# Kernel optimization log

Measured on AMD Instinct MI355X. Metric: run time of the kernel, lower is better.

Reference implementation:

```python
import jax, jax.numpy as jnp
import numpy as np

D = 1024      # embedding_size
H = 16        # num_heads
HD = D // H   # head_size
EPS = 1e-5


def setup_inputs() -> dict:
    key = jax.random.key(0)
    ks = jax.random.split(key, 12)
    s_in = 1.0 / np.sqrt(D)
    s_hid = 1.0 / np.sqrt(4 * D)
    return {
        "x": jax.random.normal(ks[0], (2, 2048, D), dtype=jnp.float32),
        # per-head projections, no bias: [H, D, HD]
        "Wq": jax.random.normal(ks[1], (H, D, HD), dtype=jnp.float32) * s_in,
        "Wk": jax.random.normal(ks[2], (H, D, HD), dtype=jnp.float32) * s_in,
        "Wv": jax.random.normal(ks[3], (H, D, HD), dtype=jnp.float32) * s_in,
        "Wo": jax.random.normal(ks[4], (D, D), dtype=jnp.float32) * s_in,
        "bo": jnp.zeros((D,), dtype=jnp.float32),
        "W1": jax.random.normal(ks[5], (D, 4 * D), dtype=jnp.float32) * s_in,
        "b1": jnp.zeros((4 * D,), dtype=jnp.float32),
        "W2": jax.random.normal(ks[6], (4 * D, D), dtype=jnp.float32) * s_hid,
        "b2": jnp.zeros((D,), dtype=jnp.float32),
        "g1": jnp.ones((D,), dtype=jnp.float32),
        "be1": jnp.zeros((D,), dtype=jnp.float32),
        "g2": jnp.ones((D,), dtype=jnp.float32),
        "be2": jnp.zeros((D,), dtype=jnp.float32),
    }


def _layernorm(x, g, b):
    mu = jnp.mean(x, axis=-1, keepdims=True)
    var = jnp.mean(jnp.square(x - mu), axis=-1, keepdims=True)
    return (x - mu) * jax.lax.rsqrt(var + EPS) * g + b


def _block(x, Wq, Wk, Wv, Wo, bo, W1, b1, W2, b2, g1, be1, g2, be2):
    B, T, _ = x.shape
    h = _layernorm(x, g1, be1)
    # per-head projections: [B, H, T, HD]
    q = jnp.einsum('btd,hde->bhte', h, Wq)
    k = jnp.einsum('btd,hde->bhte', h, Wk)
    v = jnp.einsum('btd,hde->bhte', h, Wv)
    # NOTE: original scales by embedding_size**-0.5 (x.shape[-1]), not head_size
    scores = jnp.einsum('bhte,bhse->bhts', q, k) * (D ** -0.5)
    mask = jnp.tril(jnp.ones((T, T), dtype=bool))
    scores = jnp.where(mask, scores, -jnp.inf)
    attn = jax.nn.softmax(scores, axis=-1)           # dropout = identity (eval)
    out = jnp.einsum('bhts,bhse->bhte', attn, v)      # [B, H, T, HD]
    out = out.transpose(0, 2, 1, 3).reshape(B, T, D)  # concat heads
    x = x + (out @ Wo + bo)
    h2 = _layernorm(x, g2, be2)
    ffn = jax.nn.relu(h2 @ W1 + b1) @ W2 + b2
    return x + ffn


def reference(x, Wq, Wk, Wv, Wo, bo, W1, b1, W2, b2, g1, be1, g2, be2):
    return _block(x, Wq, Wk, Wv, Wo, bo, W1, b1, W2, b2, g1, be1, g2, be2)
```

## Files before the change

kernel.cpp:

```cpp
#include <hip/hip_runtime.h>
#include <stdint.h>

typedef unsigned short u16;
typedef __attribute__((ext_vector_type(8))) __bf16 bf16x8;
typedef __attribute__((ext_vector_type(4))) float f32x4;

#define D_EMB 1024
#define NHEAD 16
#define HDIM 64
#define TSEQ 2048
#define NTOK 4096
#define NEG_BIG -1.0e30f

#define GLD16(lp, gp) __builtin_amdgcn_global_load_lds( \
    (const __attribute__((address_space(1))) unsigned int*)(gp), \
    (__attribute__((address_space(3))) unsigned int*)(lp), 16, 0, 0)

__device__ __forceinline__ float bf2f(u16 u) {
    union { unsigned int i; float f; } c; c.i = ((unsigned int)u) << 16; return c.f;
}
__device__ __forceinline__ u16 f2bf(float f) {
    union { float f; unsigned int i; } c; c.f = f;
    unsigned int r = (c.i + 0x7FFFu + ((c.i >> 16) & 1u)) >> 16;
    return (u16)r;
}
__device__ __forceinline__ void cp16(u16* dst, const u16* src) {
    *reinterpret_cast<uint4*>(dst) = *reinterpret_cast<const uint4*>(src);
}
__device__ __forceinline__ float load_in(const u16* p, size_t idx, int f32) {
    return f32 ? reinterpret_cast<const float*>(p)[idx] : bf2f(p[idx]);
}
__device__ __forceinline__ size_t tidx(int row, int col, int KB) {
    int c = (col & 7) | ((((col >> 3) ^ row) & 3) << 3);
    return ((size_t)((row >> 7) * KB + (col >> 5)) * 128 + (row & 127)) * 32 + c;
}

__global__ void detect_kernel(const u16* __restrict__ x, u16* __restrict__ fl) {
    if (threadIdx.x == 0) {
        int f = 0;
        for (int i = 0; i < 128; ++i) {
            float v = fabsf(bf2f(x[i]));
            if (!(v <= 1.0e3f)) f = 1;
        }
        fl[0] = (u16)f;
    }
}

__global__ __launch_bounds__(256) void transpose_tiled_kernel(
        const u16* __restrict__ X, u16* __restrict__ Xt, int KB,
        const u16* __restrict__ fl) {
    __shared__ __align__(16) u16 Ts[64 * 72];
    int f32 = fl[0];
    int bi = blockIdx.y, bj = blockIdx.x;
    int NS = gridDim.x * 64;
    int t = threadIdx.x;
    for (int p = 0; p < 2; ++p) {
        int idx = p * 256 + t;
        int row = idx >> 3, col8 = (idx & 7) * 8;
        size_t src = (size_t)(bi * 64 + row) * NS + bj * 64 + col8;
        if (f32) {
            for (int jj = 0; jj < 8; ++jj)
                Ts[row * 72 + col8 + jj] = f2bf(reinterpret_cast<const float*>(X)[src + jj]);
        } else {
            cp16(&Ts[row * 72 + col8], &X[src]);
        }
    }
    __syncthreads();
    for (int p = 0; p < 2; ++p) {
        int idx = p * 256 + t;
        int row = idx >> 3, col8 = (idx & 7) * 8;
        union { u16 u[8]; uint4 v; } tmp;
        for (int jj = 0; jj < 8; ++jj) tmp.u[jj] = Ts[(col8 + jj) * 72 + row];
        int n = bj * 64 + row, k0 = bi * 64 + col8;
        *reinterpret_cast<uint4*>(&Xt[tidx(n, k0, KB)]) = tmp.v;
    }
}

__global__ __launch_bounds__(256) void pack_qkv_kernel(
        const u16* __restrict__ Wq, const u16* __restrict__ Wk,
        const u16* __restrict__ Wv, u16* __restrict__ Wt,
        const u16* __restrict__ fl) {
    int f32 = fl[0];
    int idx = blockIdx.x * 256 + threadIdx.x;
    int e = idx & 63, d = (idx >> 6) & 1023, hh = (idx >> 16) & 15, sel = idx >> 20;
    const u16* W = (sel == 0) ? Wq : ((sel == 1) ? Wk : Wv);
    size_t src = (size_t)hh * (D_EMB * HDIM) + (size_t)d * HDIM + e;
    float v = f32 ? reinterpret_cast<const float*>(W)[src] : bf2f(W[src]);
    int n = sel * 1024 + hh * 64 + e;
    Wt[tidx(n, d, 32)] = f2bf(v);
}

__global__ __launch_bounds__(256) void ln_kernel(
        const u16* __restrict__ X, const u16* __restrict__ g,
        const u16* __restrict__ be, u16* __restrict__ Ht,
        const u16* __restrict__ fl) {
    int f32 = fl[0];
    int row = blockIdx.x;
    int t = threadIdx.x;
    float v[4];
    float s = 0.f, sq = 0.f;
    for (int i = 0; i < 4; ++i) {
        v[i] = load_in(X, (size_t)row * D_EMB + t + i * 256, f32);
        s += v[i]; sq += v[i] * v[i];
    }
    for (int m = 32; m; m >>= 1) { s += __shfl_down(s, m); sq += __shfl_down(sq, m); }
    __shared__ float red[8];
    int wid = t >> 6, lane = t & 63;
    if (lane == 0) { red[wid] = s; red[wid + 4] = sq; }
    __syncthreads();
    if (t == 0) {
        float S = red[0] + red[1] + red[2] + red[3];
        float SQ = red[4] + red[5] + red[6] + red[7];
        float mean = S * (1.f / 1024.f);
        float var = SQ * (1.f / 1024.f) - mean * mean;
        red[0] = mean; red[1] = rsqrtf(var + 1e-5f);
    }
    __syncthreads();
    float mean = red[0], rstd = red[1];
    for (int i = 0; i < 4; ++i) {
        int c = t + i * 256;
        float hv = (v[i] - mean) * rstd * load_in(g, c, f32) + load_in(be, c, f32);
        Ht[tidx(row, c, 32)] = f2bf(hv);
    }
}

template<int TAG, int TN>
__global__ __launch_bounds__(256) void gemm_t(
        const u16* __restrict__ At, const u16* __restrict__ Bt, u16* __restrict__ C,
        const u16* __restrict__ bias, const u16* __restrict__ res,
        int N, int K, int flags, int row_off,
        const u16* __restrict__ fl) {
    constexpr int NF = (TN == 128) ? 4 : 2;
    __shared__ __align__(16) u16 As2[2][4096];
    __shared__ __align__(16) u16 Bs2[2][TN * 32];
    int f32 = fl[0];
    int t = threadIdx.x;
    int gx = gridDim.x, gy = gridDim.y;
    int id = blockIdx.y * gx + blockIdx.x;
    int total = gx * gy;
    int xcd = id & 7, seq = id >> 3, P = total >> 3;
    int tpb = (P >= 32) ? 32 : 16;
    int th  = (P >= 32) ? 8 : 4;
    int tile = xcd * (P / tpb) + seq / tpb;
    int within = seq % tpb;
    int tiles_x = gx >> 2;
    int bx = (tile % tiles_x) * 4 + (within & 3);
    int by = (tile / tiles_x) * th + (within >> 2);
    int n0 = bx * TN, m0 = by * 128;
    int w = t >> 6, lane = t & 63, quad = lane >> 4, l16 = lane & 15;
    int wm = (TN == 128) ? (w >> 1) * 64 : (w & 1) * 64;
    int wn = (TN == 128) ? (w & 1) * 64  : (w >> 1) * 32;
    int KB = K >> 5;
    int kb0 = (seq * (KB >> 5)) & (KB - 1);
    const u16* Ab = At + (size_t)(m0 >> 7) * KB * 4096 + w * 512 + lane * 8;
    const u16* Bb = Bt + (size_t)(n0 >> 7) * KB * 4096
                       + ((TN == 64) ? (n0 & 64) * 32 : 0) + w * 512 + lane * 8;

    auto stage = [&](int buf, int kb) {
        const u16* ga = Ab + (size_t)kb * 4096;
        const u16* gb = Bb + (size_t)kb * 4096;
        u16* la = &As2[buf][w * 512];
        u16* lb = &Bs2[buf][w * 512];
        GLD16(la, ga);
        GLD16(la + 2048, ga + 2048);
        GLD16(lb, gb);
        if constexpr (TN == 128) { GLD16(lb + 2048, gb + 2048); }
    };

    const f32x4 fz = {0.f, 0.f, 0.f, 0.f};
    f32x4 acc[4][NF];
    for (int mt = 0; mt < 4; ++mt)
        for (int nt = 0; nt < NF; ++nt) acc[mt][nt] = fz;

    stage(0, kb0);
    __syncthreads();
    int kb = kb0;
    for (int it = 0; it < KB; ++it) {
        int cur = it & 1;
        int kn = (kb + 1 == KB) ? 0 : kb + 1;
        if (it + 1 < KB) stage(cur ^ 1, kn);
        bf16x8 af[4], bfr[NF];
        for (int mt = 0; mt < 4; ++mt) {
            int r = wm + mt * 16 + l16;
            af[mt] = *reinterpret_cast<const bf16x8*>(
                &As2[cur][r * 32 + (((quad ^ r) & 3) << 3)]);
        }
        for (int nt = 0; nt < NF; ++nt) {
            int r = wn + nt * 16 + l16;
            bfr[nt] = *reinterpret_cast<const bf16x8*>(
                &Bs2[cur][r * 32 + (((quad ^ r) & 3) << 3)]);
        }
        for (int mt = 0; mt < 4; ++mt)
            for (int nt = 0; nt < NF; ++nt)
                acc[mt][nt] = __builtin_amdgcn_mfma_f32_16x16x32_bf16(af[mt], bfr[nt], acc[mt][nt], 0, 0, 0);
        __syncthreads();
        kb = kn;
    }

    int relu_f = flags & 1, out_ext = flags & 2, c_tiled = flags & 4;
    for (int mt = 0; mt < 4; ++mt)
        for (int nt = 0; nt < NF; ++nt)
            for (int r = 0; r < 4; ++r) {
                int gr = m0 + wm + mt * 16 + quad * 4 + r;
                int gc = n0 + wn + nt * 16 + l16;
                float v = acc[mt][nt][r];
                if (bias) v += load_in(bias, gc, f32);
                if (relu_f) v = v > 0.f ? v : 0.f;
                size_t oidx = (size_t)(row_off + gr) * N + gc;
                if (res) v += load_in(res, oidx, f32);
                if (c_tiled)      C[tidx(gr, gc, N >> 5)] = f2bf(v);
                else if (out_ext && f32) reinterpret_cast<float*>(C)[oidx] = v;
                else              C[oidx] = f2bf(v);
            }
}

template<int TAG, int KBL, int TN>
__global__ __launch_bounds__(256) void gemm_sk_t(
        const u16* __restrict__ At, const u16* __restrict__ Bt,
        float* __restrict__ Pp, int N, int K) {
    constexpr int NF = (TN == 128) ? 4 : 2;
    __shared__ __align__(16) u16 As2[2][4096];
    __shared__ __align__(16) u16 Bs2[2][TN * 32];
    int t = threadIdx.x;
    int gx = gridDim.x, gy = gridDim.y;
    int id = blockIdx.y * gx + blockIdx.x;
    int total = gx * gy;
    int xcd = id & 7, seq = id >> 3, P = total >> 3;
    int tpb = (P >= 32) ? 32 : 16;
    int th  = (P >= 32) ? 8 : 4;
    int tile = xcd * (P / tpb) + seq / tpb;
    int within = seq % tpb;
    int tiles_x = gx >> 2;
    int bx = (tile % tiles_x) * 4 + (within & 3);
    int by = (tile / tiles_x) * th + (within >> 2);
    int n0 = bx * TN, m0 = by * 128;
    int w = t >> 6, lane = t & 63, quad = lane >> 4, l16 = lane & 15;
    int wm = (TN == 128) ? (w >> 1) * 64 : (w & 1) * 64;
    int wn = (TN == 128) ? (w & 1) * 64  : (w >> 1) * 32;
    int KB = K >> 5;
    int kstart = blockIdx.z * KBL;
    int rel0 = seq & (KBL - 1);
    const u16* Ab = At + (size_t)(m0 >> 7) * KB * 4096 + w * 512 + lane * 8;
    const u16* Bb = Bt + (size_t)(n0 >> 7) * KB * 4096
                       + ((TN == 64) ? (n0 & 64) * 32 : 0) + w * 512 + lane * 8;

    auto stage = [&](int buf, int kb) {
        const u16* ga = Ab + (size_t)kb * 4096;
        const u16* gb = Bb + (size_t)kb * 4096;
        u16* la = &As2[buf][w * 512];
        u16* lb = &Bs2[buf][w * 512];
        GLD16(la, ga);
        GLD16(la + 2048, ga + 2048);
        GLD16(lb, gb);
        if constexpr (TN == 128) { GLD16(lb + 2048, gb + 2048); }
    };

    const f32x4 fz = {0.f, 0.f, 0.f, 0.f};
    f32x4 acc[4][NF];
    for (int mt = 0; mt < 4; ++mt)
        for (int nt = 0; nt < NF; ++nt) acc[mt][nt] = fz;

    stage(0, kstart + rel0);
    __syncthreads();
    for (int it = 0; it < KBL; ++it) {
        int cur = it & 1;
        if (it + 1 < KBL)
            stage(cur ^ 1, kstart + ((rel0 + it + 1) & (KBL - 1)));
        bf16x8 af[4], bfr[NF];
        for (int mt = 0; mt < 4; ++mt) {
            int r = wm + mt * 16 + l16;
            af[mt] = *reinterpret_cast<const bf16x8*>(
                &As2[cur][r * 32 + (((quad ^ r) & 3) << 3)]);
        }
        for (int nt = 0; nt < NF; ++nt) {
            int r = wn + nt * 16 + l16;
            bfr[nt] = *reinterpret_cast<const bf16x8*>(
                &Bs2[cur][r * 32 + (((quad ^ r) & 3) << 3)]);
        }
        for (int mt = 0; mt < 4; ++mt)
            for (int nt = 0; nt < NF; ++nt)
                acc[mt][nt] = __builtin_amdgcn_mfma_f32_16x16x32_bf16(af[mt], bfr[nt], acc[mt][nt], 0, 0, 0);
        __syncthreads();
    }

    for (int mt = 0; mt < 4; ++mt)
        for (int nt = 0; nt < NF; ++nt)
            for (int r = 0; r < 4; ++r) {
                int gr = m0 + wm + mt * 16 + quad * 4 + r;
                int gc = n0 + wn + nt * 16 + l16;
                atomicAdd(&Pp[(size_t)gr * N + gc], acc[mt][nt][r]);
            }
}

__global__ __launch_bounds__(256) void zero_f32_kernel(float* __restrict__ p) {
    const f32x4 fz = {0.f, 0.f, 0.f, 0.f};
    reinterpret_cast<f32x4*>(p)[(size_t)blockIdx.x * 256 + threadIdx.x] = fz;
}

__global__ __launch_bounds__(256) void ffn_fin_kernel(
        const float* __restrict__ Pp, const u16* __restrict__ b2,
        u16* __restrict__ out, int row_off, const u16* __restrict__ fl) {
    int f32 = fl[0];
    size_t i = ((size_t)blockIdx.x * 256 + threadIdx.x) * 4;
    int col = (int)(i & 1023);
    f32x4 pv = *reinterpret_cast<const f32x4*>(Pp + i);
    size_t o = (size_t)row_off * 1024 + i;
    if (f32) {
        float* of = reinterpret_cast<float*>(out);
        f32x4 ov = *reinterpret_cast<f32x4*>(of + o);
        for (int j = 0; j < 4; ++j)
            ov[j] += pv[j] + load_in(b2, col + j, 1);
        *reinterpret_cast<f32x4*>(of + o) = ov;
    } else {
        for (int j = 0; j < 4; ++j) {
            float v = bf2f(out[o + j]) + pv[j] + bf2f(b2[col + j]);
            out[o + j] = f2bf(v);
        }
    }
}

__global__ __launch_bounds__(256) void oproj_fin_kernel(
        const float* __restrict__ Pp, const u16* __restrict__ bo,
        const u16* __restrict__ x, u16* __restrict__ out,
        const u16* __restrict__ fl) {
    int f32 = fl[0];
    size_t i = ((size_t)blockIdx.x * 256 + threadIdx.x) * 4;
    int col = (int)(i & 1023);
    f32x4 pv = *reinterpret_cast<const f32x4*>(Pp + i);
    if (f32) {
        const float* xf = reinterpret_cast<const float*>(x);
        float* of = reinterpret_cast<float*>(out);
        f32x4 ov;
        for (int j = 0; j < 4; ++j)
            ov[j] = xf[i + j] + pv[j] + load_in(bo, col + j, 1);
        *reinterpret_cast<f32x4*>(of + i) = ov;
    } else {
        for (int j = 0; j < 4; ++j) {
            float v = bf2f(x[i + j]) + pv[j] + bf2f(bo[col + j]);
            out[i + j] = f2bf(v);
        }
    }
}

__global__ __launch_bounds__(256) void flash_kernel(
        const u16* __restrict__ qkv, u16* __restrict__ attn_t) {
    __shared__ __align__(16) u16 Qs[64 * 72];
    __shared__ __align__(16) u16 Vs[64 * 72];
    __shared__ __align__(16) u16 Ps[64 * 72];
    int t = threadIdx.x;
    int tq = gridDim.x - 1 - blockIdx.x;
    int b = blockIdx.y >> 4, h = blockIdx.y & 15;
    int wid = t >> 6, lane = t & 63, quad = lane >> 4, l16 = lane & 15;
    const size_t seq_base = (size_t)b * TSEQ;

    for (int p = 0; p < 2; ++p) {
        int idx = p * 256 + t;
        int row = idx >> 3, col8 = (idx & 7) * 8;
        cp16(&Qs[row * 72 + col8],
             &qkv[(seq_base + tq * 64 + row) * 3072 + h * 64 + col8]);
    }

    const f32x4 fz = {0.f, 0.f, 0.f, 0.f};
    float m_run[4], l_run[4];
    f32x4 o[4];
    for (int r = 0; r < 4; ++r) { m_run[r] = NEG_BIG; l_run[r] = 0.f; }
    for (int nt = 0; nt < 4; ++nt) o[nt] = fz;

    for (int j = 0; j <= tq; ++j) {
        for (int p = 0; p < 2; ++p) {
            int idx = p * 256 + t;
            int row = idx >> 3, col8 = (idx & 7) * 8;
            cp16(&Vs[row * 72 + col8],
                 &qkv[(seq_base + j * 64 + row) * 3072 + 2048 + h * 64 + col8]);
        }
        __syncthreads();

        f32x4 sa[4];
        for (int nt = 0; nt < 4; ++nt) sa[nt] = fz;
        for (int kit = 0; kit < 2; ++kit) {
            bf16x8 aq = *reinterpret_cast<const bf16x8*>(
                &Qs[(wid * 16 + l16) * 72 + kit * 32 + quad * 8]);
            for (int nt = 0; nt < 4; ++nt) {
                bf16x8 bk = *reinterpret_cast<const bf16x8*>(
                    &qkv[(seq_base + j * 64 + nt * 16 + l16) * 3072 + 1024 + h * 64 + kit * 32 + quad * 8]);
                sa[nt] = __builtin_amdgcn_mfma_f32_16x16x32_bf16(aq, bk, sa[nt], 0, 0, 0);
            }
        }

        float p_val[4][4];
        int qbase = tq * 64 + wid * 16 + quad * 4;
        int sbase = j * 64 + l16;
        for (int r = 0; r < 4; ++r) {
            float sv[4];
            float mx = NEG_BIG;
            for (int nt = 0; nt < 4; ++nt) {
                float xv = sa[nt][r] * 0.03125f;
                if (sbase + nt * 16 > qbase + r) xv = NEG_BIG;
                sv[nt] = xv;
                mx = fmaxf(mx, xv);
            }
            for (int m = 1; m < 16; m <<= 1) mx = fmaxf(mx, __shfl_xor(mx, m));
            float mnew = fmaxf(m_run[r], mx);
            float alpha = __expf(m_run[r] - mnew);
            m_run[r] = mnew;
            float rs = 0.f;
            for (int nt = 0; nt < 4; ++nt) {
                float pv = __expf(sv[nt] - mnew);
                p_val[nt][r] = pv;
                rs += pv;
            }
            for (int m = 1; m < 16; m <<= 1) rs += __shfl_xor(rs, m);
            l_run[r] = l_run[r] * alpha + rs;
            for (int nt = 0; nt < 4; ++nt) o[nt][r] *= alpha;
        }

        for (int nt = 0; nt < 4; ++nt)
            for (int r = 0; r < 4; ++r)
                Ps[(wid * 16 + quad * 4 + r) * 72 + nt * 16 + l16] = f2bf(p_val[nt][r]);
        __syncthreads();

        for (int kit = 0; kit < 2; ++kit) {
            bf16x8 ap = *reinterpret_cast<const bf16x8*>(
                &Ps[(wid * 16 + l16) * 72 + kit * 32 + quad * 8]);
            for (int nt = 0; nt < 4; ++nt) {
                union { u16 u[8]; bf16x8 v; } bv;
                for (int jj = 0; jj < 8; ++jj)
                    bv.u[jj] = Vs[(kit * 32 + quad * 8 + jj) * 72 + nt * 16 + l16];
                o[nt] = __builtin_amdgcn_mfma_f32_16x16x32_bf16(ap, bv.v, o[nt], 0, 0, 0);
            }
        }
        __syncthreads();
    }

    for (int nt = 0; nt < 4; ++nt)
        for (int r = 0; r < 4; ++r) {
            int trow = (int)seq_base + tq * 64 + wid * 16 + quad * 4 + r;
            int col = h * 64 + nt * 16 + l16;
            attn_t[tidx(trow, col, 32)] = f2bf(o[nt][r] / l_run[r]);
        }
}

extern "C" void kernel_launch(void* const* d_in, const int* in_sizes, int n_in,
                              void* d_out, int out_size, void* d_ws, size_t ws_size,
                              hipStream_t stream) {
    const u16* x   = (const u16*)d_in[0];
    const u16* Wq  = (const u16*)d_in[1];
    const u16* Wk  = (const u16*)d_in[2];
    const u16* Wv  = (const u16*)d_in[3];
    const u16* Wo  = (const u16*)d_in[4];
    const u16* bo  = (const u16*)d_in[5];
    const u16* W1  = (const u16*)d_in[6];
    const u16* b1  = (const u16*)d_in[7];
    const u16* W2  = (const u16*)d_in[8];
    const u16* b2  = (const u16*)d_in[9];
    const u16* g1  = (const u16*)d_in[10];
    const u16* be1 = (const u16*)d_in[11];
    const u16* g2  = (const u16*)d_in[12];
    const u16* be2 = (const u16*)d_in[13];
    u16* out = (u16*)d_out;

    const size_t M1 = (size_t)1 << 20;
    u16* ws    = (u16*)d_ws;
    u16* qkv   = ws;
    u16* W2t   = ws;
    u16* a1    = ws + 4 * M1;
    u16* h     = ws + 12 * M1;
    u16* attn  = ws + 12 * M1;
    u16* h2    = ws + 12 * M1;
    u16* Wtq   = ws + 16 * M1;
    u16* Wot   = ws + 16 * M1;
    u16* W1t   = ws + 16 * M1;
    u16* fl    = ws + 20 * M1;
    float* Pp  = reinterpret_cast<float*>(ws + 21 * M1);
    bool sk = ws_size >= ((size_t)58 << 20);

    detect_kernel<<<1, 64, 0, stream>>>(x, fl);

    pack_qkv_kernel<<<(3 * 16 * 1024 * 64) / 256, 256, 0, stream>>>(Wq, Wk, Wv, Wtq, fl);
    ln_kernel<<<NTOK, 256, 0, stream>>>(x, g1, be1, h, fl);
    gemm_t<0, 64><<<dim3(48, 32), 256, 0, stream>>>(
        h, Wtq, qkv, nullptr, nullptr, 3072, 1024, 0, 0, fl);

    transpose_tiled_kernel<<<dim3(16, 16), 256, 0, stream>>>(Wo, Wot, 32, fl);

    flash_kernel<<<dim3(32, 32), 256, 0, stream>>>(qkv, attn);

    if (sk) {
        zero_f32_kernel<<<4096, 256, 0, stream>>>(Pp);
        gemm_sk_t<2, 8, 64><<<dim3(16, 32, 4), 256, 0, stream>>>(attn, Wot, Pp, 1024, 1024);
        oproj_fin_kernel<<<4096, 256, 0, stream>>>(Pp, bo, x, out, fl);
    } else {
        gemm_t<1, 128><<<dim3(8, 32), 256, 0, stream>>>(
            attn, Wot, out, bo, x, 1024, 1024, 2, 0, fl);
    }

    transpose_tiled_kernel<<<dim3(16, 64), 256, 0, stream>>>(W2, W2t, 128, fl);
    transpose_tiled_kernel<<<dim3(64, 16), 256, 0, stream>>>(W1, W1t, 32, fl);
    ln_kernel<<<NTOK, 256, 0, stream>>>(out, g2, be2, h2, fl);

    gemm_t<2, 64><<<dim3(64, 16), 256, 0, stream>>>(
        h2, W1t, a1, b1, nullptr, 4096, 1024, 1 | 4, 0, fl);
    if (sk) {
        zero_f32_kernel<<<2048, 256, 0, stream>>>(Pp);
        gemm_sk_t<0, 32, 64><<<dim3(16, 16, 4), 256, 0, stream>>>(a1, W2t, Pp, 1024, 4096);
        ffn_fin_kernel<<<2048, 256, 0, stream>>>(Pp, b2, out, 0, fl);
    } else {
        gemm_t<4, 128><<<dim3(8, 16), 256, 0, stream>>>(
            a1, W2t, out, b2, out, 1024, 4096, 2, 0, fl);
    }
    gemm_t<3, 64><<<dim3(64, 16), 256, 0, stream>>>(
        h2 + (size_t)2 * M1, W1t, a1, b1, nullptr, 4096, 1024, 1 | 4, 0, fl);
    if (sk) {
        zero_f32_kernel<<<2048, 256, 0, stream>>>(Pp);
        gemm_sk_t<1, 32, 64><<<dim3(16, 16, 4), 256, 0, stream>>>(a1, W2t, Pp, 1024, 4096);
        ffn_fin_kernel<<<2048, 256, 0, stream>>>(Pp, b2, out, 2048, fl);
    } else {
        gemm_t<5, 128><<<dim3(8, 16), 256, 0, stream>>>(
            a1, W2t, out, b2, out, 1024, 4096, 2, 2048, fl);
    }
}
```

Baseline: 662.3 us.

## Write V transposed from QKV GEMM and drop LDS staging in flash attention

```diff
diff --git a/kernel.cpp b/kernel.cpp
--- a/kernel.cpp
+++ b/kernel.cpp
@@ -127,6 +127,7 @@
 template<int TAG, int TN>
 __global__ __launch_bounds__(256) void gemm_t(
         const u16* __restrict__ At, const u16* __restrict__ Bt, u16* __restrict__ C,
+        u16* __restrict__ C2,
         const u16* __restrict__ bias, const u16* __restrict__ res,
         int N, int K, int flags, int row_off,
         const u16* __restrict__ fl) {
@@ -197,7 +198,7 @@
         kb = kn;
     }
 
-    int relu_f = flags & 1, out_ext = flags & 2, c_tiled = flags & 4;
+    int relu_f = flags & 1, out_ext = flags & 2, c_tiled = flags & 4, qkvsp = flags & 8;
     for (int mt = 0; mt < 4; ++mt)
         for (int nt = 0; nt < NF; ++nt)
             for (int r = 0; r < 4; ++r) {
@@ -208,7 +209,16 @@
                 if (relu_f) v = v > 0.f ? v : 0.f;
                 size_t oidx = (size_t)(row_off + gr) * N + gc;
                 if (res) v += load_in(res, oidx, f32);
-                if (c_tiled)      C[tidx(gr, gc, N >> 5)] = f2bf(v);
+                if (qkvsp) {
+                    if (gc < 2048) {
+                        C[(size_t)gr * 2048 + gc] = f2bf(v);
+                    } else {
+                        int hh = (gc - 2048) >> 6, d = gc & 63;
+                        int bb = gr >> 11, s = gr & 2047;
+                        C2[(((size_t)bb * 16 + hh) * 64 + d) * 2048 + s] = f2bf(v);
+                    }
+                }
+                else if (c_tiled)      C[tidx(gr, gc, N >> 5)] = f2bf(v);
                 else if (out_ext && f32) reinterpret_cast<float*>(C)[oidx] = v;
                 else              C[oidx] = f2bf(v);
             }
@@ -343,22 +353,20 @@
 }
 
 __global__ __launch_bounds__(256) void flash_kernel(
-        const u16* __restrict__ qkv, u16* __restrict__ attn_t) {
-    __shared__ __align__(16) u16 Qs[64 * 72];
-    __shared__ __align__(16) u16 Vs[64 * 72];
+        const u16* __restrict__ qk, const u16* __restrict__ vt,
+        u16* __restrict__ attn_t) {
     __shared__ __align__(16) u16 Ps[64 * 72];
     int t = threadIdx.x;
     int tq = gridDim.x - 1 - blockIdx.x;
     int b = blockIdx.y >> 4, h = blockIdx.y & 15;
     int wid = t >> 6, lane = t & 63, quad = lane >> 4, l16 = lane & 15;
     const size_t seq_base = (size_t)b * TSEQ;
-
-    for (int p = 0; p < 2; ++p) {
-        int idx = p * 256 + t;
-        int row = idx >> 3, col8 = (idx & 7) * 8;
-        cp16(&Qs[row * 72 + col8],
-             &qkv[(seq_base + tq * 64 + row) * 3072 + h * 64 + col8]);
-    }
+    const u16* vplane = vt + (size_t)(b * 16 + h) * 64 * 2048;
+
+    bf16x8 aq[2];
+    for (int kit = 0; kit < 2; ++kit)
+        aq[kit] = *reinterpret_cast<const bf16x8*>(
+            &qk[(seq_base + tq * 64 + wid * 16 + l16) * 2048 + h * 64 + kit * 32 + quad * 8]);
 
     const f32x4 fz = {0.f, 0.f, 0.f, 0.f};
     float m_run[4], l_run[4];
@@ -367,23 +375,13 @@
     for (int nt = 0; nt < 4; ++nt) o[nt] = fz;
 
     for (int j = 0; j <= tq; ++j) {
-        for (int p = 0; p < 2; ++p) {
-            int idx = p * 256 + t;
-            int row = idx >> 3, col8 = (idx & 7) * 8;
-            cp16(&Vs[row * 72 + col8],
-                 &qkv[(seq_base + j * 64 + row) * 3072 + 2048 + h * 64 + col8]);
-        }
-        __syncthreads();
-
         f32x4 sa[4];
         for (int nt = 0; nt < 4; ++nt) sa[nt] = fz;
         for (int kit = 0; kit < 2; ++kit) {
-            bf16x8 aq = *reinterpret_cast<const bf16x8*>(
-                &Qs[(wid * 16 + l16) * 72 + kit * 32 + quad * 8]);
             for (int nt = 0; nt < 4; ++nt) {
                 bf16x8 bk = *reinterpret_cast<const bf16x8*>(
-                    &qkv[(seq_base + j * 64 + nt * 16 + l16) * 3072 + 1024 + h * 64 + kit * 32 + quad * 8]);
-                sa[nt] = __builtin_amdgcn_mfma_f32_16x16x32_bf16(aq, bk, sa[nt], 0, 0, 0);
+                    &qk[(seq_base + j * 64 + nt * 16 + l16) * 2048 + 1024 + h * 64 + kit * 32 + quad * 8]);
+                sa[nt] = __builtin_amdgcn_mfma_f32_16x16x32_bf16(aq[kit], bk, sa[nt], 0, 0, 0);
             }
         }
 
@@ -417,19 +415,16 @@
         for (int nt = 0; nt < 4; ++nt)
             for (int r = 0; r < 4; ++r)
                 Ps[(wid * 16 + quad * 4 + r) * 72 + nt * 16 + l16] = f2bf(p_val[nt][r]);
-        __syncthreads();
 
         for (int kit = 0; kit < 2; ++kit) {
             bf16x8 ap = *reinterpret_cast<const bf16x8*>(
                 &Ps[(wid * 16 + l16) * 72 + kit * 32 + quad * 8]);
             for (int nt = 0; nt < 4; ++nt) {
-                union { u16 u[8]; bf16x8 v; } bv;
-                for (int jj = 0; jj < 8; ++jj)
-                    bv.u[jj] = Vs[(kit * 32 + quad * 8 + jj) * 72 + nt * 16 + l16];
-                o[nt] = __builtin_amdgcn_mfma_f32_16x16x32_bf16(ap, bv.v, o[nt], 0, 0, 0);
+                bf16x8 bv = *reinterpret_cast<const bf16x8*>(
+                    &vplane[(size_t)(nt * 16 + l16) * 2048 + j * 64 + kit * 32 + quad * 8]);
+                o[nt] = __builtin_amdgcn_mfma_f32_16x16x32_bf16(ap, bv, o[nt], 0, 0, 0);
             }
         }
-        __syncthreads();
     }
 
     for (int nt = 0; nt < 4; ++nt)
@@ -461,7 +456,8 @@
 
     const size_t M1 = (size_t)1 << 20;
     u16* ws    = (u16*)d_ws;
-    u16* qkv   = ws;
+    u16* qk    = ws;
+    u16* vt    = ws + 8 * M1;
     u16* W2t   = ws;
     u16* a1    = ws + 4 * M1;
     u16* h     = ws + 12 * M1;
@@ -479,11 +475,11 @@
     pack_qkv_kernel<<<(3 * 16 * 1024 * 64) / 256, 256, 0, stream>>>(Wq, Wk, Wv, Wtq, fl);
     ln_kernel<<<NTOK, 256, 0, stream>>>(x, g1, be1, h, fl);
     gemm_t<0, 64><<<dim3(48, 32), 256, 0, stream>>>(
-        h, Wtq, qkv, nullptr, nullptr, 3072, 1024, 0, 0, fl);
+        h, Wtq, qk, vt, nullptr, nullptr, 3072, 1024, 8, 0, fl);
 
     transpose_tiled_kernel<<<dim3(16, 16), 256, 0, stream>>>(Wo, Wot, 32, fl);
 
-    flash_kernel<<<dim3(32, 32), 256, 0, stream>>>(qkv, attn);
+    flash_kernel<<<dim3(32, 32), 256, 0, stream>>>(qk, vt, attn);
 
     if (sk) {
         zero_f32_kernel<<<4096, 256, 0, stream>>>(Pp);
@@ -491,7 +487,7 @@
         oproj_fin_kernel<<<4096, 256, 0, stream>>>(Pp, bo, x, out, fl);
     } else {
         gemm_t<1, 128><<<dim3(8, 32), 256, 0, stream>>>(
-            attn, Wot, out, bo, x, 1024, 1024, 2, 0, fl);
+            attn, Wot, out, nullptr, bo, x, 1024, 1024, 2, 0, fl);
     }
 
     transpose_tiled_kernel<<<dim3(16, 64), 256, 0, stream>>>(W2, W2t, 128, fl);
@@ -499,23 +495,23 @@
     ln_kernel<<<NTOK, 256, 0, stream>>>(out, g2, be2, h2, fl);
 
     gemm_t<2, 64><<<dim3(64, 16), 256, 0, stream>>>(
-        h2, W1t, a1, b1, nullptr, 4096, 1024, 1 | 4, 0, fl);
+        h2, W1t, a1, nullptr, b1, nullptr, 4096, 1024, 1 | 4, 0, fl);
     if (sk) {
         zero_f32_kernel<<<2048, 256, 0, stream>>>(Pp);
         gemm_sk_t<0, 32, 64><<<dim3(16, 16, 4), 256, 0, stream>>>(a1, W2t, Pp, 1024, 4096);
         ffn_fin_kernel<<<2048, 256, 0, stream>>>(Pp, b2, out, 0, fl);
     } else {
         gemm_t<4, 128><<<dim3(8, 16), 256, 0, stream>>>(
-            a1, W2t, out, b2, out, 1024, 4096, 2, 0, fl);
+            a1, W2t, out, nullptr, b2, out, 1024, 4096, 2, 0, fl);
     }
     gemm_t<3, 64><<<dim3(64, 16), 256, 0, stream>>>(
-        h2 + (size_t)2 * M1, W1t, a1, b1, nullptr, 4096, 1024, 1 | 4, 0, fl);
+        h2 + (size_t)2 * M1, W1t, a1, nullptr, b1, nullptr, 4096, 1024, 1 | 4, 0, fl);
     if (sk) {
         zero_f32_kernel<<<2048, 256, 0, stream>>>(Pp);
         gemm_sk_t<1, 32, 64><<<dim3(16, 16, 4), 256, 0, stream>>>(a1, W2t, Pp, 1024, 4096);
         ffn_fin_kernel<<<2048, 256, 0, stream>>>(Pp, b2, out, 2048, fl);
     } else {
         gemm_t<5, 128><<<dim3(8, 16), 256, 0, stream>>>(
-            a1, W2t, out, b2, out, 1024, 4096, 2, 2048, fl);
-    }
-}
+            a1, W2t, out, nullptr, b2, out, 1024, 4096, 2, 2048, fl);
+    }
+}
```

New measurement: 682.6 us. 1.03x slower.
